# Optimization experiments

Hardware: AMD Instinct MI355X
Metric: run time of the kernel (lower is better)

## Reference

```python
import jax, jax.numpy as jnp
import numpy as np

IMAGE_DIM = (1000, 1000)   # (width, height) as used by the torch module
PATCH_SIZE = 5
NUM_TERMS = 10
NUM_PATCHES = (IMAGE_DIM[0] // PATCH_SIZE) * (IMAGE_DIM[1] // PATCH_SIZE)


def setup_inputs() -> dict:
    key = jax.random.key(0)
    k1, k2 = jax.random.split(key, 2)
    num_pixels = IMAGE_DIM[0] * IMAGE_DIM[1]
    pix_coord = jax.random.uniform(k1, (num_pixels, 2), dtype=jnp.float32)
    # xavier_uniform on [num_patches, 3, num_terms, 2]: fan_in=num_terms, fan_out=2 (last two dims)
    bound = float(np.sqrt(6.0 / (NUM_TERMS + 2)))
    coefficients = jax.random.uniform(
        k2, (NUM_PATCHES, 3, NUM_TERMS, 2), dtype=jnp.float32,
        minval=-bound, maxval=bound)
    bias = jnp.zeros((NUM_PATCHES, 3), dtype=jnp.float32)
    return {"pix_coord": pix_coord, "coefficients": coefficients, "bias": bias}


def reference(pix_coord, coefficients, bias):
    width = IMAGE_DIM[0]
    num_pixels = pix_coord.shape[0]
    idx = jnp.arange(num_pixels, dtype=jnp.int32)
    row = idx // width
    col = idx % width
    patch_idx = (row // PATCH_SIZE) * (width // PATCH_SIZE) + col // PATCH_SIZE  # [N]
    powers = jnp.arange(NUM_TERMS, dtype=jnp.float32)                            # [T]
    # Vandermonde in each coordinate: [N, 2, T]
    vand = pix_coord[:, :, None] ** powers
    cg = coefficients[patch_idx]   # [N, 3, T, 2]
    bg = bias[patch_idx]           # [N, 3]
    # sum_d sum_t coeff[n,c,t,d] * pix[n,d]^t  + bias  -> output [3, N]
    out = jnp.einsum('nctd,ndt->cn', cg, vand) + bg.T
    return out
```

## Files before the change

### kernel.cpp

```cpp
#include <hip/hip_runtime.h>

constexpr int WIDTH     = 1000;
constexpr int HEIGHT    = 1000;
constexpr int N_PIXELS  = WIDTH * HEIGHT;
constexpr int PATCH     = 5;
constexpr int PATCHES_X = WIDTH / PATCH;
constexpr int BLOCK     = 256;
constexpr int MAXP      = BLOCK / PATCH + 2;

__global__ __launch_bounds__(256) void ts_approx_kernel(
    const float* __restrict__ pix,
    const float* __restrict__ coef,
    const float* __restrict__ bias,
    float* __restrict__ out)
{
    __shared__ float scoef[MAXP * 60];
    __shared__ float sbias[MAXP * 3];

    const int tid  = threadIdx.x;
    const int prow = blockIdx.y;
    const int c0   = blockIdx.x * BLOCK;
    const int p0   = c0 / PATCH;
    const int pend = min(c0 + BLOCK - 1, WIDTH - 1) / PATCH;
    const int np   = pend - p0 + 1;

    const float4* g4 = reinterpret_cast<const float4*>(coef + (size_t)(prow * PATCHES_X + p0) * 60);
    float4* s4 = reinterpret_cast<float4*>(scoef);
    const int nf4 = np * 15;
    for (int j = tid; j < nf4; j += BLOCK) s4[j] = g4[j];
    const float* gb = bias + (size_t)(prow * PATCHES_X + p0) * 3;
    for (int j = tid; j < np * 3; j += BLOCK) sbias[j] = gb[j];
    __syncthreads();

    const int col = c0 + tid;
    if (col >= WIDTH) return;

    const int row0 = prow * PATCH;
    const int pl   = col / PATCH - p0;

    float4 cf[15];
    const float4* c4 = reinterpret_cast<const float4*>(scoef + pl * 60);
    #pragma unroll
    for (int i = 0; i < 15; ++i) cf[i] = c4[i];
    const float b0 = sbias[pl * 3 + 0];
    const float b1 = sbias[pl * 3 + 1];
    const float b2 = sbias[pl * 3 + 2];

    const float2* p2 = reinterpret_cast<const float2*>(pix);

    #pragma unroll
    for (int r = 0; r < PATCH; ++r) {
        const int n = (row0 + r) * WIDTH + col;
        const float2 p = p2[n];
        const float x = p.x, y = p.y;

        float a0 = b0, a1 = b1, a2 = b2;
        float xt = 1.0f, yt = 1.0f;
        #pragma unroll
        for (int i = 0; i < 5; ++i) {
            const float xt1 = xt * x, yt1 = yt * y;
            float4 v = cf[i];
            a0 = fmaf(v.x, xt,  a0); a0 = fmaf(v.y, yt,  a0);
            a0 = fmaf(v.z, xt1, a0); a0 = fmaf(v.w, yt1, a0);
            v = cf[5 + i];
            a1 = fmaf(v.x, xt,  a1); a1 = fmaf(v.y, yt,  a1);
            a1 = fmaf(v.z, xt1, a1); a1 = fmaf(v.w, yt1, a1);
            v = cf[10 + i];
            a2 = fmaf(v.x, xt,  a2); a2 = fmaf(v.y, yt,  a2);
            a2 = fmaf(v.z, xt1, a2); a2 = fmaf(v.w, yt1, a2);
            xt = xt1 * x; yt = yt1 * y;
        }

        out[0 * N_PIXELS + n] = a0;
        out[1 * N_PIXELS + n] = a1;
        out[2 * N_PIXELS + n] = a2;
    }
}

extern "C" void kernel_launch(void* const* d_in, const int* in_sizes, int n_in,
                              void* d_out, int out_size, void* d_ws, size_t ws_size,
                              hipStream_t stream) {
    const float* pix  = (const float*)d_in[0];
    const float* coef = (const float*)d_in[1];
    const float* bias = (const float*)d_in[2];
    float* out = (float*)d_out;

    dim3 grid((WIDTH + BLOCK - 1) / BLOCK, HEIGHT / PATCH);
    ts_approx_kernel<<<grid, BLOCK, 0, stream>>>(pix, coef, bias, out);
}
```

Measured before the change: 11.72 us.

## Use Horner evaluation, preload pixel rows, and shrink blocks to one wavefront

Replaces the power-accumulation polynomial evaluation with Horner's scheme per coordinate, which removes the running power multiplies. All five pixel-row loads are hoisted ahead of the compute so they can be in flight together. The block size drops from 256 to 64 threads, giving many more blocks to spread across CUs, and the shared patch buffer is resized to match. Smaller blocks add redundant coefficient staging at block edges and change the launch geometry.

```diff
diff --git a/kernel.cpp b/kernel.cpp
--- a/kernel.cpp
+++ b/kernel.cpp
@@ -5,10 +5,10 @@
 constexpr int N_PIXELS  = WIDTH * HEIGHT;
 constexpr int PATCH     = 5;
 constexpr int PATCHES_X = WIDTH / PATCH;
-constexpr int BLOCK     = 256;
-constexpr int MAXP      = BLOCK / PATCH + 2;
+constexpr int BLOCK     = 64;
+constexpr int MAXP      = BLOCK / PATCH + 3;
 
-__global__ __launch_bounds__(256) void ts_approx_kernel(
+__global__ __launch_bounds__(64) void ts_approx_kernel(
     const float* __restrict__ pix,
     const float* __restrict__ coef,
     const float* __restrict__ bias,
@@ -48,32 +48,35 @@
 
     const float2* p2 = reinterpret_cast<const float2*>(pix);
 
+    float2 p[PATCH];
+    #pragma unroll
+    for (int r = 0; r < PATCH; ++r) p[r] = p2[(row0 + r) * WIDTH + col];
+
     #pragma unroll
     for (int r = 0; r < PATCH; ++r) {
+        const float x = p[r].x, y = p[r].y;
         const int n = (row0 + r) * WIDTH + col;
-        const float2 p = p2[n];
-        const float x = p.x, y = p.y;
 
-        float a0 = b0, a1 = b1, a2 = b2;
-        float xt = 1.0f, yt = 1.0f;
+        float res[3];
         #pragma unroll
-        for (int i = 0; i < 5; ++i) {
-            const float xt1 = xt * x, yt1 = yt * y;
-            float4 v = cf[i];
-            a0 = fmaf(v.x, xt,  a0); a0 = fmaf(v.y, yt,  a0);
-            a0 = fmaf(v.z, xt1, a0); a0 = fmaf(v.w, yt1, a0);
-            v = cf[5 + i];
-            a1 = fmaf(v.x, xt,  a1); a1 = fmaf(v.y, yt,  a1);
-            a1 = fmaf(v.z, xt1, a1); a1 = fmaf(v.w, yt1, a1);
-            v = cf[10 + i];
-            a2 = fmaf(v.x, xt,  a2); a2 = fmaf(v.y, yt,  a2);
-            a2 = fmaf(v.z, xt1, a2); a2 = fmaf(v.w, yt1, a2);
-            xt = xt1 * x; yt = yt1 * y;
+        for (int c = 0; c < 3; ++c) {
+            const int b = 5 * c;
+            float hx = cf[b + 4].z;
+            float hy = cf[b + 4].w;
+            hx = fmaf(hx, x, cf[b + 4].x);  hy = fmaf(hy, y, cf[b + 4].y);
+            hx = fmaf(hx, x, cf[b + 3].z);  hy = fmaf(hy, y, cf[b + 3].w);
+            hx = fmaf(hx, x, cf[b + 3].x);  hy = fmaf(hy, y, cf[b + 3].y);
+            hx = fmaf(hx, x, cf[b + 2].z);  hy = fmaf(hy, y, cf[b + 2].w);
+            hx = fmaf(hx, x, cf[b + 2].x);  hy = fmaf(hy, y, cf[b + 2].y);
+            hx = fmaf(hx, x, cf[b + 1].z);  hy = fmaf(hy, y, cf[b + 1].w);
+            hx = fmaf(hx, x, cf[b + 1].x);  hy = fmaf(hy, y, cf[b + 1].y);
+            hx = fmaf(hx, x, cf[b + 0].z);  hy = fmaf(hy, y, cf[b + 0].w);
+            hx = fmaf(hx, x, cf[b + 0].x);  hy = fmaf(hy, y, cf[b + 0].y);
+            res[c] = hx + hy;
         }
-
-        out[0 * N_PIXELS + n] = a0;
-        out[1 * N_PIXELS + n] = a1;
-        out[2 * N_PIXELS + n] = a2;
+        out[0 * N_PIXELS + n] = res[0] + b0;
+        out[1 * N_PIXELS + n] = res[1] + b1;
+        out[2 * N_PIXELS + n] = res[2] + b2;
     }
 }
 
```

Result: no change. 11.87 us (+1.3%).
